# Performance work log

Measured on AMD Instinct MI355X. Metric: run time of the kernel, lower is better.

The kernel has to match this reference:

```python
import jax, jax.numpy as jnp
import numpy as np
import math
from jax import lax

DIM = 96
D_MODEL = 2 * DIM            # SS2D d_model
D_INNER = 2 * D_MODEL        # expand = 2
D_STATE = 16
DT_RANK = math.ceil(D_MODEL / 16)
K = 4
B_, H_, W_ = 2, 48, 48


def setup_inputs() -> dict:
    key = jax.random.key(0)
    ks = jax.random.split(key, 12)
    r = lambda k, s, sc=0.02: jax.random.normal(k, s, jnp.float32) * sc
    A = np.tile(np.arange(1, D_STATE + 1, dtype=np.float32)[None, :], (K * D_INNER, 1))
    return dict(
        x=jax.random.normal(ks[0], (B_, DIM, H_, W_), jnp.float32),
        w_init=r(ks[1], (D_MODEL, DIM)),
        b_init=r(ks[2], (D_MODEL,)),
        w_fina=r(ks[3], (DIM, D_MODEL)),
        b_fina=r(ks[4], (DIM,)),
        in_proj_w=r(ks[5], (2 * D_INNER, D_MODEL)),
        conv_w=r(ks[6], (D_INNER, 1, 3, 3), 0.1),
        conv_b=r(ks[7], (D_INNER,)),
        x_proj_w=r(ks[8], (K, DT_RANK + 2 * D_STATE, D_INNER)),
        dt_w=r(ks[9], (K, D_INNER, DT_RANK), 0.1),
        dt_b=r(ks[10], (K, D_INNER), 0.1),
        A_logs=jnp.asarray(np.log(A)),
        Ds=jnp.ones((K * D_INNER,), jnp.float32),
        ln_g=jnp.ones((D_INNER,), jnp.float32),
        ln_b=jnp.zeros((D_INNER,), jnp.float32),
        out_proj_w=r(ks[11], (D_MODEL, D_INNER)),
    )


def _gelu(x):
    return jax.nn.gelu(x, approximate=False)


def _conv1x1(x, w, b):
    # x: (b,c,h,w), w: (o,c)
    return jnp.einsum('oc,bchw->bohw', w, x) + b[None, :, None, None]


def _ss2d(x, in_proj_w, conv_w, conv_b, x_proj_w, dt_w, dt_b, A_logs, Ds, ln_g, ln_b, out_proj_w):
    # x: (b, h, w, d_model)
    b, h, w, _ = x.shape
    L = h * w
    xz = jnp.einsum('bhwc,oc->bhwo', x, in_proj_w)          # (b,h,w,2*d_inner)
    xx, z = jnp.split(xz, 2, axis=-1)
    xc = xx.transpose(0, 3, 1, 2)                            # (b, d_inner, h, w)
    xc = lax.conv_general_dilated(xc, conv_w, (1, 1), 'SAME',
                                  feature_group_count=D_INNER,
                                  dimension_numbers=('NCHW', 'OIHW', 'NCHW'))
    xc = jax.nn.silu(xc + conv_b[None, :, None, None])
    # 4 scan directions: hw, wh, reversed hw, reversed wh
    x_hw = xc.reshape(b, D_INNER, L)
    x_wh = xc.transpose(0, 1, 3, 2).reshape(b, D_INNER, L)
    xs = jnp.stack([x_hw, x_wh, x_hw[..., ::-1], x_wh[..., ::-1]], axis=1)   # (b,K,d,L)
    x_dbl = jnp.einsum('bkdl,kcd->bkcl', xs, x_proj_w)
    dts = x_dbl[:, :, :DT_RANK]                               # (b,K,r,L)
    Bs = x_dbl[:, :, DT_RANK:DT_RANK + D_STATE]               # (b,K,n,L)
    Cs = x_dbl[:, :, DT_RANK + D_STATE:]                      # (b,K,n,L)
    dts = jnp.einsum('bkrl,kdr->bkdl', dts, dt_w)
    delta = jax.nn.softplus(dts + dt_b[None, :, :, None])     # (b,K,d,L)
    A = -jnp.exp(A_logs).reshape(K, D_INNER, D_STATE)         # (K,d,n)
    Dm = Ds.reshape(K, D_INNER)
    # selective scan over L (time-major stacked inputs)
    u_t = xs.transpose(3, 0, 1, 2)      # (L,b,K,d)
    dt_t = delta.transpose(3, 0, 1, 2)  # (L,b,K,d)
    B_t = Bs.transpose(3, 0, 1, 2)      # (L,b,K,n)
    C_t = Cs.transpose(3, 0, 1, 2)      # (L,b,K,n)
    h0 = jnp.zeros((b, K, D_INNER, D_STATE), xs.dtype)

    def step(hst, inp):
        u, dt, Bv, Cv = inp
        dA = jnp.exp(dt[..., None] * A)                       # (b,K,d,n)
        hst = dA * hst + (dt * u)[..., None] * Bv[:, :, None, :]
        y = jnp.einsum('bkdn,bkn->bkd', hst, Cv)
        return hst, y

    _, ys = lax.scan(step, h0, (u_t, dt_t, B_t, C_t))         # (L,b,K,d)
    ys = ys.transpose(1, 2, 3, 0) + Dm[None, :, :, None] * xs  # (b,K,d,L)
    y1 = ys[:, 0]
    y3 = ys[:, 2][..., ::-1]
    y2 = ys[:, 1].reshape(b, D_INNER, w, h).transpose(0, 1, 3, 2).reshape(b, D_INNER, L)
    y4 = ys[:, 3][..., ::-1].reshape(b, D_INNER, w, h).transpose(0, 1, 3, 2).reshape(b, D_INNER, L)
    y = (y1 + y2 + y3 + y4).transpose(0, 2, 1).reshape(b, h, w, D_INNER)
    mu = y.mean(-1, keepdims=True)
    var = y.var(-1, keepdims=True)
    y = (y - mu) / jnp.sqrt(var + 1e-5) * ln_g + ln_b
    y = y * jax.nn.silu(z)
    return jnp.einsum('bhwd,od->bhwo', y, out_proj_w)         # (b,h,w,d_model)


def _forward(x, w_init, b_init, w_fina, b_fina, in_proj_w, conv_w, conv_b,
             x_proj_w, dt_w, dt_b, A_logs, Ds, ln_g, ln_b, out_proj_w):
    x1 = _gelu(_conv1x1(x, w_init, b_init))                   # (b,2*dim,h,w)
    x0 = x1
    xt = x1.transpose(0, 2, 3, 1)                             # b h w c
    y = _ss2d(xt, in_proj_w, conv_w, conv_b, x_proj_w, dt_w, dt_b,
              A_logs, Ds, ln_g, ln_b, out_proj_w)
    y = y.transpose(0, 3, 1, 2)
    return _gelu(_conv1x1(y + x0, w_fina, b_fina))            # (b,dim,h,w)


def reference(x, w_init, b_init, w_fina, b_fina, in_proj_w, conv_w, conv_b,
              x_proj_w, dt_w, dt_b, A_logs, Ds, ln_g, ln_b, out_proj_w):
    return _forward(x, w_init, b_init, w_fina, b_fina, in_proj_w, conv_w, conv_b,
                    x_proj_w, dt_w, dt_b, A_logs, Ds, ln_g, ln_b, out_proj_w)
```

## Files before the change

### kernel.cpp

```cpp
#include <hip/hip_runtime.h>
#include <math.h>

#define LL 2304
#define HH 48
#define WW 48
#define BB 2
#define CI 96
#define DM 192
#define DI 384
#define KK 4
#define RR 12
#define NN 16
#define KC 44
#define CH 96
#define LEN 24

typedef short bf16x8 __attribute__((ext_vector_type(8)));
typedef float f32x4 __attribute__((ext_vector_type(4)));

__device__ __forceinline__ float gelu_f(float x){
    return 0.5f*x*(1.0f+erff(x*0.70710678118654752f));
}
__device__ __forceinline__ float silu_f(float x){
    return x/(1.0f+__expf(-x));
}
__device__ __forceinline__ float softplus_f(float x){
    return fmaxf(x,0.0f) + log1pf(__expf(-fabsf(x)));
}
__device__ __forceinline__ unsigned short bf16_rne(float x){
    unsigned u = __float_as_uint(x);
    unsigned r = (u + 0x7FFFu + ((u>>16)&1u)) >> 16;
    return (unsigned short)r;
}
__device__ __forceinline__ void split_bf16(float x, unsigned short& h, unsigned short& l){
    h = bf16_rne(x);
    float fh = __uint_as_float(((unsigned)h)<<16);
    l = bf16_rne(x - fh);
}

template<int C, int OT>
__device__ __forceinline__ void gemmN_acc(const float* __restrict__ xb, const float* __restrict__ w,
        int o0, float* wl, float acc[OT], int tid){
    for(int idx=tid; idx<OT*C; idx+=256) wl[idx] = w[(size_t)o0*C + idx];
    __syncthreads();
    #pragma unroll 2
    for(int c=0;c<C;c+=4){
        float x0=xb[(size_t)(c+0)*LL], x1=xb[(size_t)(c+1)*LL];
        float x2=xb[(size_t)(c+2)*LL], x3=xb[(size_t)(c+3)*LL];
        #pragma unroll
        for(int o=0;o<OT;o++){
            float4 wq = *reinterpret_cast<const float4*>(wl + o*C + c);
            acc[o] = fmaf(wq.x,x0, fmaf(wq.y,x1, fmaf(wq.z,x2, fmaf(wq.w,x3, acc[o]))));
        }
    }
}

__global__ __launch_bounds__(256) void k_convw(const float* __restrict__ ipw, const float* __restrict__ xpw,
        const float* __restrict__ opw, short* __restrict__ wh_ip, short* __restrict__ wl_ip,
        short* __restrict__ wh_xp, short* __restrict__ wl_xp,
        short* __restrict__ wh_op, short* __restrict__ wl_op){
    int idx = blockIdx.x*256 + threadIdx.x;
    unsigned short h, l;
    if(idx < 147456){
        split_bf16(ipw[idx], h, l); wh_ip[idx]=h; wl_ip[idx]=l;
    } else if(idx < 147456+67584){
        int j = idx - 147456;
        split_bf16(xpw[j], h, l); wh_xp[j]=h; wl_xp[j]=l;
    } else {
        int j = idx - 215040;
        split_bf16(opw[j], h, l); wh_op[j]=h; wl_op[j]=l;
    }
}

template<int K>
__device__ __forceinline__ void mfma_core(const short* __restrict__ Ah, const short* __restrict__ Al,
        const short* __restrict__ Bh, const short* __restrict__ Bl, f32x4 acc[2][4]){
    int lane = threadIdx.x & 63;
    int rl = lane & 15, g = lane >> 4;
    #pragma unroll
    for(int kc=0; kc<K; kc+=32){
        bf16x8 ah[2], al[2], bh[4], bl[4];
        #pragma unroll
        for(int mi=0;mi<2;mi++){
            ah[mi] = *reinterpret_cast<const bf16x8*>(Ah + (size_t)(mi*16+rl)*K + kc + g*8);
            al[mi] = *reinterpret_cast<const bf16x8*>(Al + (size_t)(mi*16+rl)*K + kc + g*8);
        }
        #pragma unroll
        for(int ni=0;ni<4;ni++){
            bh[ni] = *reinterpret_cast<const bf16x8*>(Bh + (size_t)(ni*16+rl)*K + kc + g*8);
            bl[ni] = *reinterpret_cast<const bf16x8*>(Bl + (size_t)(ni*16+rl)*K + kc + g*8);
        }
        #pragma unroll
        for(int mi=0;mi<2;mi++){
            #pragma unroll
            for(int ni=0;ni<4;ni++){
                acc[mi][ni] = __builtin_amdgcn_mfma_f32_16x16x32_bf16(ah[mi], bh[ni], acc[mi][ni], 0,0,0);
                acc[mi][ni] = __builtin_amdgcn_mfma_f32_16x16x32_bf16(ah[mi], bl[ni], acc[mi][ni], 0,0,0);
                acc[mi][ni] = __builtin_amdgcn_mfma_f32_16x16x32_bf16(al[mi], bh[ni], acc[mi][ni], 0,0,0);
            }
        }
    }
}

__global__ __launch_bounds__(256) void k_init(const float* __restrict__ x, const float* __restrict__ w,
        const float* __restrict__ bias, float* __restrict__ x1,
        short* __restrict__ x1Th, short* __restrict__ x1Tl){
    __shared__ float wl[8*CI];
    int l = blockIdx.x*256 + threadIdx.x;
    int o0 = blockIdx.y*8; int b = blockIdx.z;
    float acc[8];
    #pragma unroll
    for(int j=0;j<8;j++) acc[j] = bias[o0+j];
    gemmN_acc<CI,8>(x + (size_t)b*CI*LL + l, w, o0, wl, acc, threadIdx.x);
    float* ob = x1 + (size_t)b*DM*LL + o0*LL + l;
    unsigned hw[4], lw[4];
    #pragma unroll
    for(int j=0;j<8;j+=2){
        float g0 = gelu_f(acc[j]), g1 = gelu_f(acc[j+1]);
        ob[j*LL] = g0; ob[(j+1)*LL] = g1;
        unsigned short h0,l0,h1,l1;
        split_bf16(g0,h0,l0); split_bf16(g1,h1,l1);
        hw[j>>1] = (unsigned)h0 | ((unsigned)h1<<16);
        lw[j>>1] = (unsigned)l0 | ((unsigned)l1<<16);
    }
    size_t tbase = ((size_t)b*LL + l)*DM + o0;
    *reinterpret_cast<uint4*>(x1Th + tbase) = make_uint4(hw[0],hw[1],hw[2],hw[3]);
    *reinterpret_cast<uint4*>(x1Tl + tbase) = make_uint4(lw[0],lw[1],lw[2],lw[3]);
}

__global__ __launch_bounds__(256) void k_inproj(const short* __restrict__ wh, const short* __restrict__ wlo,
        const short* __restrict__ x1Th, const short* __restrict__ x1Tl,
        float* __restrict__ xx, float* __restrict__ z){
    int w = threadIdx.x >> 6, lane = threadIdx.x & 63;
    int wm = w >> 1, wn = w & 1;
    int m0 = blockIdx.y*64 + wm*32;
    int n0 = blockIdx.x*128 + wn*64;
    int b = blockIdx.z;
    f32x4 acc[2][4];
    #pragma unroll
    for(int mi=0;mi<2;mi++)
        #pragma unroll
        for(int ni=0;ni<4;ni++) acc[mi][ni] = (f32x4){0.f,0.f,0.f,0.f};
    mfma_core<DM>(wh + (size_t)m0*DM, wlo + (size_t)m0*DM,
                  x1Th + ((size_t)b*LL + n0)*DM, x1Tl + ((size_t)b*LL + n0)*DM, acc);
    int rl = lane & 15, g = lane >> 4;
    #pragma unroll
    for(int mi=0;mi<2;mi++){
        #pragma unroll
        for(int ni=0;ni<4;ni++){
            #pragma unroll
            for(int i=0;i<4;i++){
                int m = m0 + mi*16 + g*4 + i;
                int l = n0 + ni*16 + rl;
                float v = acc[mi][ni][i];
                if(m < DI) xx[((size_t)b*DI + m)*LL + l] = v;
                else       z [((size_t)b*DI + (m-DI))*LL + l] = v;
            }
        }
    }
}

__global__ __launch_bounds__(256) void k_dwconv(const float* __restrict__ xx, const float* __restrict__ cw,
        const float* __restrict__ cb, float* __restrict__ xc){
    int l = blockIdx.x*256 + threadIdx.x;
    int d = blockIdx.y; int b = blockIdx.z;
    int h = l/WW, w = l%WW;
    const float* src = xx + ((size_t)b*DI + d)*LL;
    float acc = cb[d];
    #pragma unroll
    for(int dh=-1;dh<=1;dh++){
        int hh = h+dh; if(hh<0||hh>=HH) continue;
        #pragma unroll
        for(int dw=-1;dw<=1;dw++){
            int w2 = w+dw; if(w2<0||w2>=WW) continue;
            acc += cw[d*9 + (dh+1)*3 + (dw+1)] * src[hh*WW + w2];
        }
    }
    xc[((size_t)b*DI + d)*LL + l] = silu_f(acc);
}

__global__ __launch_bounds__(256) void k_transpose(const float* __restrict__ xc, const float* __restrict__ z,
        float* __restrict__ xcT, float* __restrict__ zT,
        short* __restrict__ xcTh, short* __restrict__ xcTl){
    __shared__ float tile[32][33];
    int which = blockIdx.z >> 1;
    int b = blockIdx.z & 1;
    const float* src = which ? z : xc;
    float* dst = which ? zT : xcT;
    int l0 = blockIdx.x*32, d0 = blockIdx.y*32;
    int tx = threadIdx.x & 31, ty = threadIdx.x >> 5;
    #pragma unroll
    for(int j=0;j<4;j++)
        tile[ty+8*j][tx] = src[((size_t)b*DI + d0+ty+8*j)*LL + l0+tx];
    __syncthreads();
    #pragma unroll
    for(int j=0;j<4;j++){
        float v = tile[tx][ty+8*j];
        size_t di = ((size_t)b*LL + l0+ty+8*j)*DI + d0+tx;
        dst[di] = v;
        if(!which){
            unsigned short h,l;
            split_bf16(v,h,l);
            xcTh[di] = (short)h; xcTl[di] = (short)l;
        }
    }
}

__global__ __launch_bounds__(256) void k_proj(const short* __restrict__ wh, const short* __restrict__ wlo,
        const short* __restrict__ xcTh, const short* __restrict__ xcTl,
        float* __restrict__ pj){
    int w = threadIdx.x >> 6, lane = threadIdx.x & 63;
    int wm = w >> 1, wn = w & 1;
    int m0 = blockIdx.y*64 + wm*32;
    int n0 = blockIdx.x*128 + wn*64;
    int b = blockIdx.z;
    f32x4 acc[2][4];
    #pragma unroll
    for(int mi=0;mi<2;mi++)
        #pragma unroll
        for(int ni=0;ni<4;ni++) acc[mi][ni] = (f32x4){0.f,0.f,0.f,0.f};
    mfma_core<DI>(wh + (size_t)m0*DI, wlo + (size_t)m0*DI,
                  xcTh + ((size_t)b*LL + n0)*DI, xcTl + ((size_t)b*LL + n0)*DI, acc);
    int rl = lane & 15, g = lane >> 4;
    #pragma unroll
    for(int mi=0;mi<2;mi++){
        #pragma unroll
        for(int ni=0;ni<4;ni++){
            #pragma unroll
            for(int i=0;i<4;i++){
                int m = m0 + mi*16 + g*4 + i;
                if(m >= KK*KC) continue;
                int l = n0 + ni*16 + rl;
                pj[((size_t)b*(KK*KC) + m)*LL + l] = acc[mi][ni][i];
            }
        }
    }
}

__global__ __launch_bounds__(256) void k_delta(const float* __restrict__ pj, const float* __restrict__ dtw,
        const float* __restrict__ dtb, float* __restrict__ deltaT){
    __shared__ float pjs[RR*32];
    int p0 = blockIdx.x*32;
    int bk = blockIdx.z; int b = bk>>2, k = bk&3;
    int lane = threadIdx.x & 63, sub = threadIdx.x >> 6;
    int d = blockIdx.y*64 + lane;
    const float* pjb = pj + ((size_t)b*(KK*KC) + k*KC)*LL;
    for(int idx=threadIdx.x; idx<RR*32; idx+=256){
        int r = idx>>5, pp = idx&31;
        pjs[idx] = pjb[(size_t)r*LL + p0+pp];
    }
    __syncthreads();
    float wr[RR];
    #pragma unroll
    for(int r=0;r<RR;r++) wr[r] = dtw[((size_t)k*DI + d)*RR + r];
    float dtbv = dtb[k*DI + d];
    #pragma unroll
    for(int i=0;i<8;i++){
        int pp = sub*8+i;
        float acc = dtbv;
        #pragma unroll
        for(int r=0;r<RR;r++) acc += wr[r]*pjs[r*32+pp];
        deltaT[((size_t)bk*LL + p0+pp)*DI + d] = softplus_f(acc);
    }
}

__device__ __forceinline__ int perm_pos(int k, int l){
    int lk = (k>=2) ? (LL-1-l) : l;
    return (k&1) ? ((lk%WW)*WW + lk/WW) : lk;
}

__global__ __launch_bounds__(384) void k_scan1(const float* __restrict__ xcT, const float* __restrict__ pj,
        const float* __restrict__ deltaT, const float* __restrict__ alogs,
        float* __restrict__ gbuf, float* __restrict__ Sbuf){
    __shared__ float bs[LEN*16];
    int chunk = blockIdx.x;
    int bk = blockIdx.y; int b = bk>>2, k = bk&3;
    int lane = threadIdx.x & 63, wv = threadIdx.x >> 6;
    int d = wv*64 + lane;
    const float* pjb = pj + ((size_t)b*(KK*KC) + k*KC)*LL;
    for(int idx=threadIdx.x; idx<LEN*16; idx+=384){
        int s = idx>>4, n = idx&15;
        int p = perm_pos(k, chunk*LEN+s);
        bs[idx] = pjb[(size_t)(RR+n)*LL + p];
    }
    __syncthreads();
    float a[NN], h[NN];
    #pragma unroll
    for(int n=0;n<NN;n++){ a[n] = -__expf(alogs[((size_t)k*DI + d)*NN + n]); h[n]=0.f; }
    float S = 0.f;
    const float* dptr = deltaT + (size_t)bk*LL*DI + d;
    const float* uptr = xcT + (size_t)b*LL*DI + d;
    for(int s=0;s<LEN;s++){
        int p = perm_pos(k, chunk*LEN+s);
        float dt = dptr[(size_t)p*DI];
        float u  = uptr[(size_t)p*DI];
        S += dt;
        float du = dt*u;
        #pragma unroll
        for(int nq=0;nq<4;nq++){
            float4 Bq = *reinterpret_cast<const float4*>(bs + s*16 + nq*4);
            h[nq*4+0] = __expf(dt*a[nq*4+0])*h[nq*4+0] + du*Bq.x;
            h[nq*4+1] = __expf(dt*a[nq*4+1])*h[nq*4+1] + du*Bq.y;
            h[nq*4+2] = __expf(dt*a[nq*4+2])*h[nq*4+2] + du*Bq.z;
            h[nq*4+3] = __expf(dt*a[nq*4+3])*h[nq*4+3] + du*Bq.w;
        }
    }
    int base = (bk*CH + chunk)*NN;
    #pragma unroll
    for(int n=0;n<NN;n++) gbuf[(size_t)(base+n)*DI + d] = h[n];
    Sbuf[(size_t)(bk*CH + chunk)*DI + d] = S;
}

__global__ __launch_bounds__(256) void k_scan2(const float* __restrict__ alogs, const float* __restrict__ Sbuf,
        float* __restrict__ gbuf){
    int id = blockIdx.x*256 + threadIdx.x;
    int d = id % DI;
    int n = (id/DI) % NN;
    int bk = id/(DI*NN);
    int k = bk & 3;
    float a = -__expf(alogs[((size_t)k*DI + d)*NN + n]);
    float h = 0.f;
    for(int j=0;j<CH;j++){
        float S = Sbuf[(size_t)(bk*CH + j)*DI + d];
        size_t gi = (size_t)((bk*CH + j)*NN + n)*DI + d;
        float g = gbuf[gi];
        gbuf[gi] = h;
        h = __expf(a*S)*h + g;
    }
}

__global__ __launch_bounds__(384) void k_scan3(const float* __restrict__ xcT, const float* __restrict__ pj,
        const float* deltaT, const float* __restrict__ alogs,
        const float* __restrict__ gbuf, float* yout){
    __shared__ float bs[LEN*32];
    int chunk = blockIdx.x;
    int bk = blockIdx.y; int b = bk>>2, k = bk&3;
    int lane = threadIdx.x & 63, wv = threadIdx.x >> 6;
    int d = wv*64 + lane;
    const float* pjb = pj + ((size_t)b*(KK*KC) + k*KC)*LL;
    for(int idx=threadIdx.x; idx<LEN*32; idx+=384){
        int s = idx>>5, c = idx&31;
        int p = perm_pos(k, chunk*LEN+s);
        bs[idx] = pjb[(size_t)(RR+c)*LL + p];
    }
    __syncthreads();
    float a[NN], h[NN];
    int base = (bk*CH + chunk)*NN;
    #pragma unroll
    for(int n=0;n<NN;n++){
        a[n] = -__expf(alogs[((size_t)k*DI + d)*NN + n]);
        h[n] = gbuf[(size_t)(base+n)*DI + d];
    }
    const float* dptr = deltaT + (size_t)bk*LL*DI + d;
    const float* uptr = xcT + (size_t)b*LL*DI + d;
    float* yptr = yout + (size_t)bk*LL*DI + d;
    for(int s=0;s<LEN;s++){
        int p = perm_pos(k, chunk*LEN+s);
        float dt = dptr[(size_t)p*DI];
        float u  = uptr[(size_t)p*DI];
        float du = dt*u;
        float y = 0.f;
        #pragma unroll
        for(int nq=0;nq<4;nq++){
            float4 Bq = *reinterpret_cast<const float4*>(bs + s*32 + nq*4);
            float4 Cq = *reinterpret_cast<const float4*>(bs + s*32 + 16 + nq*4);
            h[nq*4+0] = __expf(dt*a[nq*4+0])*h[nq*4+0] + du*Bq.x;  y += h[nq*4+0]*Cq.x;
            h[nq*4+1] = __expf(dt*a[nq*4+1])*h[nq*4+1] + du*Bq.y;  y += h[nq*4+1]*Cq.y;
            h[nq*4+2] = __expf(dt*a[nq*4+2])*h[nq*4+2] + du*Bq.z;  y += h[nq*4+2]*Cq.z;
            h[nq*4+3] = __expf(dt*a[nq*4+3])*h[nq*4+3] + du*Bq.w;  y += h[nq*4+3]*Cq.w;
        }
        yptr[(size_t)p*DI] = y;
    }
}

__global__ __launch_bounds__(256) void k_merge(const float* __restrict__ yout, const float* __restrict__ xcT,
        const float* __restrict__ zT, const float* __restrict__ Ds,
        const float* __restrict__ lng, const float* __restrict__ lnb,
        short* __restrict__ ygh, short* __restrict__ ygl){
    __shared__ float tile[32*385];
    int p0 = blockIdx.x*32; int b = blockIdx.y;
    for(int idx=threadIdx.x; idx<32*DI; idx+=256){
        int pp = idx/DI, d = idx%DI; int p = p0+pp;
        float dsum = Ds[d] + Ds[DI+d] + Ds[2*DI+d] + Ds[3*DI+d];
        float v = dsum * xcT[((size_t)b*LL + p)*DI + d];
        #pragma unroll
        for(int kk=0;kk<4;kk++) v += yout[((size_t)(b*4+kk)*LL + p)*DI + d];
        tile[pp*385 + d] = v;
    }
    __syncthreads();
    int lane = threadIdx.x & 63, wv = threadIdx.x >> 6;
    for(int i=0;i<8;i++){
        int pp = wv*8 + i; int p = p0+pp;
        float s1=0.f, s2=0.f;
        float vals[6];
        #pragma unroll
        for(int j=0;j<6;j++){ float v = tile[pp*385 + lane + 64*j]; vals[j]=v; s1+=v; s2+=v*v; }
        #pragma unroll
        for(int m=1;m<64;m<<=1){ s1 += __shfl_xor(s1,m); s2 += __shfl_xor(s2,m); }
        float mu = s1*(1.0f/DI);
        float var = s2*(1.0f/DI) - mu*mu;
        float rstd = rsqrtf(var + 1e-5f);
        #pragma unroll
        for(int j=0;j<6;j++){
            int c = lane + 64*j;
            float zv = zT[((size_t)b*LL + p)*DI + c];
            float y = (vals[j]-mu)*rstd*lng[c] + lnb[c];
            float gv = y * silu_f(zv);
            unsigned short h,l;
            split_bf16(gv,h,l);
            size_t oi = ((size_t)b*LL + p)*DI + c;
            ygh[oi] = (short)h; ygl[oi] = (short)l;
        }
    }
}

__global__ __launch_bounds__(256) void k_outproj(const short* __restrict__ wh, const short* __restrict__ wlo,
        const short* __restrict__ ygh, const short* __restrict__ ygl,
        const float* __restrict__ x1, float* __restrict__ yo){
    int w = threadIdx.x >> 6, lane = threadIdx.x & 63;
    int wm = w >> 1, wn = w & 1;
    int m0 = blockIdx.y*64 + wm*32;
    int n0 = blockIdx.x*128 + wn*64;
    int b = blockIdx.z;
    f32x4 acc[2][4];
    #pragma unroll
    for(int mi=0;mi<2;mi++)
        #pragma unroll
        for(int ni=0;ni<4;ni++) acc[mi][ni] = (f32x4){0.f,0.f,0.f,0.f};
    mfma_core<DI>(wh + (size_t)m0*DI, wlo + (size_t)m0*DI,
                  ygh + ((size_t)b*LL + n0)*DI, ygl + ((size_t)b*LL + n0)*DI, acc);
    int rl = lane & 15, g = lane >> 4;
    #pragma unroll
    for(int mi=0;mi<2;mi++){
        #pragma unroll
        for(int ni=0;ni<4;ni++){
            #pragma unroll
            for(int i=0;i<4;i++){
                int m = m0 + mi*16 + g*4 + i;
                int l = n0 + ni*16 + rl;
                size_t oi = ((size_t)b*DM + m)*LL + l;
                yo[oi] = acc[mi][ni][i] + x1[oi];
            }
        }
    }
}

__global__ __launch_bounds__(256) void k_final(const float* __restrict__ yo,
        const float* __restrict__ w, const float* __restrict__ bias, float* __restrict__ out){
    __shared__ float wl[4*DM];
    int l = blockIdx.x*256 + threadIdx.x;
    int o0 = blockIdx.y*4; int b = blockIdx.z;
    float acc[4];
    #pragma unroll
    for(int j=0;j<4;j++) acc[j] = bias[o0+j];
    gemmN_acc<DM,4>(yo + (size_t)b*DM*LL + l, w, o0, wl, acc, threadIdx.x);
    float* ob = out + (size_t)b*CI*LL + o0*LL + l;
    #pragma unroll
    for(int j=0;j<4;j++) ob[j*LL] = gelu_f(acc[j]);
}

extern "C" void kernel_launch(void* const* d_in, const int* in_sizes, int n_in,
                              void* d_out, int out_size, void* d_ws, size_t ws_size,
                              hipStream_t stream) {
    const float* x        = (const float*)d_in[0];
    const float* w_init   = (const float*)d_in[1];
    const float* b_init   = (const float*)d_in[2];
    const float* w_fina   = (const float*)d_in[3];
    const float* b_fina   = (const float*)d_in[4];
    const float* in_proj_w= (const float*)d_in[5];
    const float* conv_w   = (const float*)d_in[6];
    const float* conv_b   = (const float*)d_in[7];
    const float* x_proj_w = (const float*)d_in[8];
    const float* dt_w     = (const float*)d_in[9];
    const float* dt_b     = (const float*)d_in[10];
    const float* A_logs   = (const float*)d_in[11];
    const float* Ds       = (const float*)d_in[12];
    const float* ln_g     = (const float*)d_in[13];
    const float* ln_b     = (const float*)d_in[14];
    const float* out_proj_w=(const float*)d_in[15];

    float* ws = (float*)d_ws;
    float* x1   = ws;
    float* xx   = x1 + 884736;
    float* z    = xx + 1769472;
    float* xc   = z  + 1769472;
    float* xcT  = xc + 1769472;
    float* zT   = xcT+ 1769472;
    float* pj   = zT + 1769472;
    float* deltaT = pj + 811008;
    float* wcvt = deltaT + 7077888;

    short* wh_ip = (short*)wcvt;
    short* wl_ip = wh_ip + 147456;
    short* wh_xp = wl_ip + 147456;
    short* wl_xp = wh_xp + 73728;
    short* wh_op = wl_xp + 73728;
    short* wl_op = wh_op + 73728;

    short* x1Th = (short*)deltaT;
    short* x1Tl = x1Th + 884736;
    short* xcTh = x1Tl + 884736;
    short* xcTl = xcTh + 1769472;

    float* gbuf = xx;
    float* Sbuf = xx + 4718592;
    float* yout = deltaT;
    short* ygh  = (short*)xc;
    short* ygl  = ygh + 1769472;
    float* yo   = z;

    dim3 blk(256);
    k_convw  <<<dim3(1128), blk, 0, stream>>>(in_proj_w, x_proj_w, out_proj_w,
                                              wh_ip, wl_ip, wh_xp, wl_xp, wh_op, wl_op);
    k_init   <<<dim3(9,24,BB), blk, 0, stream>>>(x, w_init, b_init, x1, x1Th, x1Tl);
    k_inproj <<<dim3(18,12,BB), blk, 0, stream>>>(wh_ip, wl_ip, x1Th, x1Tl, xx, z);
    k_dwconv <<<dim3(9,DI,BB), blk, 0, stream>>>(xx, conv_w, conv_b, xc);
    k_transpose<<<dim3(72,12,2*BB), blk, 0, stream>>>(xc, z, xcT, zT, xcTh, xcTl);
    k_proj   <<<dim3(18,3,BB), blk, 0, stream>>>(wh_xp, wl_xp, xcTh, xcTl, pj);
    k_delta  <<<dim3(72,6,BB*KK), blk, 0, stream>>>(pj, dt_w, dt_b, deltaT);
    k_scan1  <<<dim3(CH,BB*KK), dim3(384), 0, stream>>>(xcT, pj, deltaT, A_logs, gbuf, Sbuf);
    k_scan2  <<<dim3(192), blk, 0, stream>>>(A_logs, Sbuf, gbuf);
    k_scan3  <<<dim3(CH,BB*KK), dim3(384), 0, stream>>>(xcT, pj, deltaT, A_logs, gbuf, yout);
    k_merge  <<<dim3(72,BB), blk, 0, stream>>>(yout, xcT, zT, Ds, ln_g, ln_b, ygh, ygl);
    k_outproj<<<dim3(18,3,BB), blk, 0, stream>>>(wh_op, wl_op, ygh, ygl, x1, yo);
    k_final  <<<dim3(9,24,BB), blk, 0, stream>>>(yo, w_fina, b_fina, (float*)d_out);
}
```

Baseline: 325.1 us.

## Fuse delta projection into scans and move init/final convs to split-bf16 MFMA

Removes the separate k_delta kernel and its large deltaT buffer. Each scan chunk now loads the dt-rank projection rows into shared memory and recomputes dt plus softplus inline, in both scan1 and scan3. The init and final 1x1 convolutions become split-bf16 MFMA GEMMs, using a new transpose kernel for x and having outproj write the transposed bf16 hi/lo residual sum directly. The aim is to cut memory traffic and slow fp32 FMA GEMMs, at the cost of duplicated dt work across the two scan passes, an extra launch, and a rearranged workspace.

Result: slower. 353.6 us (+8.8%).

```diff
diff --git a/kernel.cpp b/kernel.cpp
--- a/kernel.cpp
+++ b/kernel.cpp
@@ -38,37 +38,30 @@
     l = bf16_rne(x - fh);
 }
 
-template<int C, int OT>
-__device__ __forceinline__ void gemmN_acc(const float* __restrict__ xb, const float* __restrict__ w,
-        int o0, float* wl, float acc[OT], int tid){
-    for(int idx=tid; idx<OT*C; idx+=256) wl[idx] = w[(size_t)o0*C + idx];
-    __syncthreads();
-    #pragma unroll 2
-    for(int c=0;c<C;c+=4){
-        float x0=xb[(size_t)(c+0)*LL], x1=xb[(size_t)(c+1)*LL];
-        float x2=xb[(size_t)(c+2)*LL], x3=xb[(size_t)(c+3)*LL];
-        #pragma unroll
-        for(int o=0;o<OT;o++){
-            float4 wq = *reinterpret_cast<const float4*>(wl + o*C + c);
-            acc[o] = fmaf(wq.x,x0, fmaf(wq.y,x1, fmaf(wq.z,x2, fmaf(wq.w,x3, acc[o]))));
-        }
-    }
-}
-
 __global__ __launch_bounds__(256) void k_convw(const float* __restrict__ ipw, const float* __restrict__ xpw,
-        const float* __restrict__ opw, short* __restrict__ wh_ip, short* __restrict__ wl_ip,
+        const float* __restrict__ opw, const float* __restrict__ wiw, const float* __restrict__ wfw,
+        short* __restrict__ wh_ip, short* __restrict__ wl_ip,
         short* __restrict__ wh_xp, short* __restrict__ wl_xp,
-        short* __restrict__ wh_op, short* __restrict__ wl_op){
+        short* __restrict__ wh_op, short* __restrict__ wl_op,
+        short* __restrict__ wh_in, short* __restrict__ wl_in,
+        short* __restrict__ wh_fi, short* __restrict__ wl_fi){
     int idx = blockIdx.x*256 + threadIdx.x;
+    if(idx >= 325632) return;
     unsigned short h, l;
     if(idx < 147456){
         split_bf16(ipw[idx], h, l); wh_ip[idx]=h; wl_ip[idx]=l;
-    } else if(idx < 147456+67584){
+    } else if(idx < 215040){
         int j = idx - 147456;
         split_bf16(xpw[j], h, l); wh_xp[j]=h; wl_xp[j]=l;
-    } else {
+    } else if(idx < 288768){
         int j = idx - 215040;
         split_bf16(opw[j], h, l); wh_op[j]=h; wl_op[j]=l;
+    } else if(idx < 307200){
+        int j = idx - 288768;
+        split_bf16(wiw[j], h, l); wh_in[j]=h; wl_in[j]=l;
+    } else {
+        int j = idx - 307200;
+        split_bf16(wfw[j], h, l); wh_fi[j]=h; wl_fi[j]=l;
     }
 }
 
@@ -102,30 +95,63 @@
     }
 }
 
-__global__ __launch_bounds__(256) void k_init(const float* __restrict__ x, const float* __restrict__ w,
-        const float* __restrict__ bias, float* __restrict__ x1,
-        short* __restrict__ x1Th, short* __restrict__ x1Tl){
-    __shared__ float wl[8*CI];
-    int l = blockIdx.x*256 + threadIdx.x;
-    int o0 = blockIdx.y*8; int b = blockIdx.z;
-    float acc[8];
-    #pragma unroll
-    for(int j=0;j<8;j++) acc[j] = bias[o0+j];
-    gemmN_acc<CI,8>(x + (size_t)b*CI*LL + l, w, o0, wl, acc, threadIdx.x);
-    float* ob = x1 + (size_t)b*DM*LL + o0*LL + l;
-    unsigned hw[4], lw[4];
-    #pragma unroll
-    for(int j=0;j<8;j+=2){
-        float g0 = gelu_f(acc[j]), g1 = gelu_f(acc[j+1]);
-        ob[j*LL] = g0; ob[(j+1)*LL] = g1;
-        unsigned short h0,l0,h1,l1;
-        split_bf16(g0,h0,l0); split_bf16(g1,h1,l1);
-        hw[j>>1] = (unsigned)h0 | ((unsigned)h1<<16);
-        lw[j>>1] = (unsigned)l0 | ((unsigned)l1<<16);
-    }
-    size_t tbase = ((size_t)b*LL + l)*DM + o0;
-    *reinterpret_cast<uint4*>(x1Th + tbase) = make_uint4(hw[0],hw[1],hw[2],hw[3]);
-    *reinterpret_cast<uint4*>(x1Tl + tbase) = make_uint4(lw[0],lw[1],lw[2],lw[3]);
+__global__ __launch_bounds__(256) void k_xT(const float* __restrict__ x,
+        short* __restrict__ xTh, short* __restrict__ xTl){
+    __shared__ float tile[32][33];
+    int b = blockIdx.z;
+    int l0 = blockIdx.x*32, c0 = blockIdx.y*32;
+    int tx = threadIdx.x & 31, ty = threadIdx.x >> 5;
+    #pragma unroll
+    for(int j=0;j<4;j++)
+        tile[ty+8*j][tx] = x[((size_t)b*CI + c0+ty+8*j)*LL + l0+tx];
+    __syncthreads();
+    #pragma unroll
+    for(int j=0;j<4;j++){
+        float v = tile[tx][ty+8*j];
+        size_t di = ((size_t)b*LL + l0+ty+8*j)*CI + c0+tx;
+        unsigned short h,l; split_bf16(v,h,l);
+        xTh[di]=(short)h; xTl[di]=(short)l;
+    }
+}
+
+__global__ __launch_bounds__(256) void k_init(const short* __restrict__ wh, const short* __restrict__ wlo,
+        const short* __restrict__ xTh, const short* __restrict__ xTl, const float* __restrict__ bias,
+        float* __restrict__ x1, short* __restrict__ x1Th, short* __restrict__ x1Tl){
+    int w = threadIdx.x >> 6, lane = threadIdx.x & 63;
+    int wm = w >> 1, wn = w & 1;
+    int m0 = blockIdx.y*64 + wm*32;
+    int n0 = blockIdx.x*128 + wn*64;
+    int b = blockIdx.z;
+    f32x4 acc[2][4];
+    #pragma unroll
+    for(int mi=0;mi<2;mi++)
+        #pragma unroll
+        for(int ni=0;ni<4;ni++) acc[mi][ni] = (f32x4){0.f,0.f,0.f,0.f};
+    mfma_core<CI>(wh + (size_t)m0*CI, wlo + (size_t)m0*CI,
+                  xTh + ((size_t)b*LL + n0)*CI, xTl + ((size_t)b*LL + n0)*CI, acc);
+    int rl = lane & 15, g = lane >> 4;
+    #pragma unroll
+    for(int mi=0;mi<2;mi++){
+        #pragma unroll
+        for(int ni=0;ni<4;ni++){
+            int mb = m0 + mi*16 + g*4;
+            int l = n0 + ni*16 + rl;
+            unsigned hp[2], lp[2];
+            #pragma unroll
+            for(int i=0;i<4;i++){
+                int m = mb + i;
+                float v = gelu_f(acc[mi][ni][i] + bias[m]);
+                x1[((size_t)b*DM + m)*LL + l] = v;
+                unsigned short h, lo_;
+                split_bf16(v, h, lo_);
+                if(i & 1){ hp[i>>1] |= ((unsigned)h)<<16; lp[i>>1] |= ((unsigned)lo_)<<16; }
+                else     { hp[i>>1] = h; lp[i>>1] = lo_; }
+            }
+            size_t tb = ((size_t)b*LL + l)*DM + mb;
+            *reinterpret_cast<uint2*>(x1Th + tb) = make_uint2(hp[0],hp[1]);
+            *reinterpret_cast<uint2*>(x1Tl + tb) = make_uint2(lp[0],lp[1]);
+        }
+    }
 }
 
 __global__ __launch_bounds__(256) void k_inproj(const short* __restrict__ wh, const short* __restrict__ wlo,
@@ -237,42 +263,16 @@
     }
 }
 
-__global__ __launch_bounds__(256) void k_delta(const float* __restrict__ pj, const float* __restrict__ dtw,
-        const float* __restrict__ dtb, float* __restrict__ deltaT){
-    __shared__ float pjs[RR*32];
-    int p0 = blockIdx.x*32;
-    int bk = blockIdx.z; int b = bk>>2, k = bk&3;
-    int lane = threadIdx.x & 63, sub = threadIdx.x >> 6;
-    int d = blockIdx.y*64 + lane;
-    const float* pjb = pj + ((size_t)b*(KK*KC) + k*KC)*LL;
-    for(int idx=threadIdx.x; idx<RR*32; idx+=256){
-        int r = idx>>5, pp = idx&31;
-        pjs[idx] = pjb[(size_t)r*LL + p0+pp];
-    }
-    __syncthreads();
-    float wr[RR];
-    #pragma unroll
-    for(int r=0;r<RR;r++) wr[r] = dtw[((size_t)k*DI + d)*RR + r];
-    float dtbv = dtb[k*DI + d];
-    #pragma unroll
-    for(int i=0;i<8;i++){
-        int pp = sub*8+i;
-        float acc = dtbv;
-        #pragma unroll
-        for(int r=0;r<RR;r++) acc += wr[r]*pjs[r*32+pp];
-        deltaT[((size_t)bk*LL + p0+pp)*DI + d] = softplus_f(acc);
-    }
-}
-
 __device__ __forceinline__ int perm_pos(int k, int l){
     int lk = (k>=2) ? (LL-1-l) : l;
     return (k&1) ? ((lk%WW)*WW + lk/WW) : lk;
 }
 
 __global__ __launch_bounds__(384) void k_scan1(const float* __restrict__ xcT, const float* __restrict__ pj,
-        const float* __restrict__ deltaT, const float* __restrict__ alogs,
+        const float* __restrict__ dtw, const float* __restrict__ dtb, const float* __restrict__ alogs,
         float* __restrict__ gbuf, float* __restrict__ Sbuf){
     __shared__ float bs[LEN*16];
+    __shared__ float dls[LEN*RR];
     int chunk = blockIdx.x;
     int bk = blockIdx.y; int b = bk>>2, k = bk&3;
     int lane = threadIdx.x & 63, wv = threadIdx.x >> 6;
@@ -283,16 +283,27 @@
         int p = perm_pos(k, chunk*LEN+s);
         bs[idx] = pjb[(size_t)(RR+n)*LL + p];
     }
+    for(int idx=threadIdx.x; idx<LEN*RR; idx+=384){
+        int s = idx/RR, r = idx - s*RR;
+        int p = perm_pos(k, chunk*LEN+s);
+        dls[idx] = pjb[(size_t)r*LL + p];
+    }
     __syncthreads();
+    float wr[RR];
+    #pragma unroll
+    for(int r=0;r<RR;r++) wr[r] = dtw[((size_t)k*DI + d)*RR + r];
+    float dtbv = dtb[k*DI + d];
     float a[NN], h[NN];
     #pragma unroll
     for(int n=0;n<NN;n++){ a[n] = -__expf(alogs[((size_t)k*DI + d)*NN + n]); h[n]=0.f; }
     float S = 0.f;
-    const float* dptr = deltaT + (size_t)bk*LL*DI + d;
     const float* uptr = xcT + (size_t)b*LL*DI + d;
     for(int s=0;s<LEN;s++){
         int p = perm_pos(k, chunk*LEN+s);
-        float dt = dptr[(size_t)p*DI];
+        float dtraw = dtbv;
+        #pragma unroll
+        for(int r=0;r<RR;r++) dtraw += wr[r]*dls[s*RR+r];
+        float dt = softplus_f(dtraw);
         float u  = uptr[(size_t)p*DI];
         S += dt;
         float du = dt*u;
@@ -330,9 +341,10 @@
 }
 
 __global__ __launch_bounds__(384) void k_scan3(const float* __restrict__ xcT, const float* __restrict__ pj,
-        const float* deltaT, const float* __restrict__ alogs,
-        const float* __restrict__ gbuf, float* yout){
+        const float* __restrict__ dtw, const float* __restrict__ dtb, const float* __restrict__ alogs,
+        const float* __restrict__ gbuf, float* __restrict__ yout){
     __shared__ float bs[LEN*32];
+    __shared__ float dls[LEN*RR];
     int chunk = blockIdx.x;
     int bk = blockIdx.y; int b = bk>>2, k = bk&3;
     int lane = threadIdx.x & 63, wv = threadIdx.x >> 6;
@@ -343,7 +355,16 @@
         int p = perm_pos(k, chunk*LEN+s);
         bs[idx] = pjb[(size_t)(RR+c)*LL + p];
     }
+    for(int idx=threadIdx.x; idx<LEN*RR; idx+=384){
+        int s = idx/RR, r = idx - s*RR;
+        int p = perm_pos(k, chunk*LEN+s);
+        dls[idx] = pjb[(size_t)r*LL + p];
+    }
     __syncthreads();
+    float wr[RR];
+    #pragma unroll
+    for(int r=0;r<RR;r++) wr[r] = dtw[((size_t)k*DI + d)*RR + r];
+    float dtbv = dtb[k*DI + d];
     float a[NN], h[NN];
     int base = (bk*CH + chunk)*NN;
     #pragma unroll
@@ -351,12 +372,14 @@
         a[n] = -__expf(alogs[((size_t)k*DI + d)*NN + n]);
         h[n] = gbuf[(size_t)(base+n)*DI + d];
     }
-    const float* dptr = deltaT + (size_t)bk*LL*DI + d;
     const float* uptr = xcT + (size_t)b*LL*DI + d;
     float* yptr = yout + (size_t)bk*LL*DI + d;
     for(int s=0;s<LEN;s++){
         int p = perm_pos(k, chunk*LEN+s);
-        float dt = dptr[(size_t)p*DI];
+        float dtraw = dtbv;
+        #pragma unroll
+        for(int r=0;r<RR;r++) dtraw += wr[r]*dls[s*RR+r];
+        float dt = softplus_f(dtraw);
         float u  = uptr[(size_t)p*DI];
         float du = dt*u;
         float y = 0.f;
@@ -416,7 +439,7 @@
 
 __global__ __launch_bounds__(256) void k_outproj(const short* __restrict__ wh, const short* __restrict__ wlo,
         const short* __restrict__ ygh, const short* __restrict__ ygl,
-        const float* __restrict__ x1, float* __restrict__ yo){
+        const float* __restrict__ x1, short* __restrict__ yoTh, short* __restrict__ yoTl){
     int w = threadIdx.x >> 6, lane = threadIdx.x & 63;
     int wm = w >> 1, wn = w & 1;
     int m0 = blockIdx.y*64 + wm*32;
@@ -434,29 +457,54 @@
     for(int mi=0;mi<2;mi++){
         #pragma unroll
         for(int ni=0;ni<4;ni++){
+            int mb = m0 + mi*16 + g*4;
+            int l = n0 + ni*16 + rl;
+            unsigned hp[2], lp[2];
+            #pragma unroll
+            for(int i=0;i<4;i++){
+                int m = mb + i;
+                float v = acc[mi][ni][i] + x1[((size_t)b*DM + m)*LL + l];
+                unsigned short h, lo_;
+                split_bf16(v, h, lo_);
+                if(i & 1){ hp[i>>1] |= ((unsigned)h)<<16; lp[i>>1] |= ((unsigned)lo_)<<16; }
+                else     { hp[i>>1] = h; lp[i>>1] = lo_; }
+            }
+            size_t tb = ((size_t)b*LL + l)*DM + mb;
+            *reinterpret_cast<uint2*>(yoTh + tb) = make_uint2(hp[0],hp[1]);
+            *reinterpret_cast<uint2*>(yoTl + tb) = make_uint2(lp[0],lp[1]);
+        }
+    }
+}
+
+__global__ __launch_bounds__(256) void k_final(const short* __restrict__ wh, const short* __restrict__ wlo,
+        const short* __restrict__ yoTh, const short* __restrict__ yoTl, const float* __restrict__ bias,
+        float* __restrict__ out){
+    int w = threadIdx.x >> 6, lane = threadIdx.x & 63;
+    int wm = w >> 1, wn = w & 1;
+    int m0 = blockIdx.y*64 + wm*32;
+    int n0 = blockIdx.x*128 + wn*64;
+    int b = blockIdx.z;
+    f32x4 acc[2][4];
+    #pragma unroll
+    for(int mi=0;mi<2;mi++)
+        #pragma unroll
+        for(int ni=0;ni<4;ni++) acc[mi][ni] = (f32x4){0.f,0.f,0.f,0.f};
+    mfma_core<DM>(wh + (size_t)m0*DM, wlo + (size_t)m0*DM,
+                  yoTh + ((size_t)b*LL + n0)*DM, yoTl + ((size_t)b*LL + n0)*DM, acc);
+    int rl = lane & 15, g = lane >> 4;
+    #pragma unroll
+    for(int mi=0;mi<2;mi++){
+        #pragma unroll
+        for(int ni=0;ni<4;ni++){
             #pragma unroll
             for(int i=0;i<4;i++){
                 int m = m0 + mi*16 + g*4 + i;
+                if(m >= CI) continue;
                 int l = n0 + ni*16 + rl;
-                size_t oi = ((size_t)b*DM + m)*LL + l;
-                yo[oi] = acc[mi][ni][i] + x1[oi];
+                out[((size_t)b*CI + m)*LL + l] = gelu_f(acc[mi][ni][i] + bias[m]);
             }
         }
     }
-}
-
-__global__ __launch_bounds__(256) void k_final(const float* __restrict__ yo,
-        const float* __restrict__ w, const float* __restrict__ bias, float* __restrict__ out){
-    __shared__ float wl[4*DM];
-    int l = blockIdx.x*256 + threadIdx.x;
-    int o0 = blockIdx.y*4; int b = blockIdx.z;
-    float acc[4];
-    #pragma unroll
-    for(int j=0;j<4;j++) acc[j] = bias[o0+j];
-    gemmN_acc<DM,4>(yo + (size_t)b*DM*LL + l, w, o0, wl, acc, threadIdx.x);
-    float* ob = out + (size_t)b*CI*LL + o0*LL + l;
-    #pragma unroll
-    for(int j=0;j<4;j++) ob[j*LL] = gelu_f(acc[j]);
 }
 
 extern "C" void kernel_launch(void* const* d_in, const int* in_sizes, int n_in,
@@ -479,7 +527,7 @@
     const float* ln_b     = (const float*)d_in[14];
     const float* out_proj_w=(const float*)d_in[15];
 
-    float* ws = (float*)d_ws;
+    float* ws   = (float*)d_ws;
     float* x1   = ws;
     float* xx   = x1 + 884736;
     float* z    = xx + 1769472;
@@ -487,41 +535,35 @@
     float* xcT  = xc + 1769472;
     float* zT   = xcT+ 1769472;
     float* pj   = zT + 1769472;
-    float* deltaT = pj + 811008;
-    float* wcvt = deltaT + 7077888;
-
-    short* wh_ip = (short*)wcvt;
-    short* wl_ip = wh_ip + 147456;
-    short* wh_xp = wl_ip + 147456;
-    short* wl_xp = wh_xp + 73728;
-    short* wh_op = wl_xp + 73728;
-    short* wl_op = wh_op + 73728;
-
-    short* x1Th = (short*)deltaT;
-    short* x1Tl = x1Th + 884736;
-    short* xcTh = x1Tl + 884736;
-    short* xcTl = xcTh + 1769472;
-
-    float* gbuf = xx;
-    float* Sbuf = xx + 4718592;
-    float* yout = deltaT;
-    short* ygh  = (short*)xc;
-    short* ygl  = ygh + 1769472;
-    float* yo   = z;
+    float* yout = pj + 811008;
+    float* gbuf = yout + 7077888;
+    float* Sbuf = gbuf + 4718592;
+    short* sb   = (short*)(Sbuf + 294912);
+    short* wh_ip = sb;            short* wl_ip = wh_ip + 147456;
+    short* wh_xp = wl_ip+147456;  short* wl_xp = wh_xp + 73728;
+    short* wh_op = wl_xp+73728;   short* wl_op = wh_op + 73728;
+    short* wh_in = wl_op+73728;   short* wl_in = wh_in + 18432;
+    short* wh_fi = wl_in+18432;   short* wl_fi = wh_fi + 18432;
+    short* xTh   = wl_fi+18432;   short* xTl   = xTh + 442368;
+    short* x1Th  = xTl+442368;    short* x1Tl  = x1Th + 884736;
+    short* xcTh  = x1Tl+884736;   short* xcTl  = xcTh + 1769472;
+    short* ygh   = xcTl+1769472;  short* ygl   = ygh + 1769472;
+    short* yoTh  = ygl+1769472;   short* yoTl  = yoTh + 884736;
 
     dim3 blk(256);
-    k_convw  <<<dim3(1128), blk, 0, stream>>>(in_proj_w, x_proj_w, out_proj_w,
-                                              wh_ip, wl_ip, wh_xp, wl_xp, wh_op, wl_op);
-    k_init   <<<dim3(9,24,BB), blk, 0, stream>>>(x, w_init, b_init, x1, x1Th, x1Tl);
+    k_convw  <<<dim3(1272), blk, 0, stream>>>(in_proj_w, x_proj_w, out_proj_w, w_init, w_fina,
+                                              wh_ip, wl_ip, wh_xp, wl_xp, wh_op, wl_op,
+                                              wh_in, wl_in, wh_fi, wl_fi);
+    k_xT     <<<dim3(72,3,BB), blk, 0, stream>>>(x, xTh, xTl);
+    k_init   <<<dim3(18,3,BB), blk, 0, stream>>>(wh_in, wl_in, xTh, xTl, b_init, x1, x1Th, x1Tl);
     k_inproj <<<dim3(18,12,BB), blk, 0, stream>>>(wh_ip, wl_ip, x1Th, x1Tl, xx, z);
     k_dwconv <<<dim3(9,DI,BB), blk, 0, stream>>>(xx, conv_w, conv_b, xc);
     k_transpose<<<dim3(72,12,2*BB), blk, 0, stream>>>(xc, z, xcT, zT, xcTh, xcTl);
     k_proj   <<<dim3(18,3,BB), blk, 0, stream>>>(wh_xp, wl_xp, xcTh, xcTl, pj);
-    k_delta  <<<dim3(72,6,BB*KK), blk, 0, stream>>>(pj, dt_w, dt_b, deltaT);
-    k_scan1  <<<dim3(CH,BB*KK), dim3(384), 0, stream>>>(xcT, pj, deltaT, A_logs, gbuf, Sbuf);
+    k_scan1  <<<dim3(CH,BB*KK), dim3(384), 0, stream>>>(xcT, pj, dt_w, dt_b, A_logs, gbuf, Sbuf);
     k_scan2  <<<dim3(192), blk, 0, stream>>>(A_logs, Sbuf, gbuf);
-    k_scan3  <<<dim3(CH,BB*KK), dim3(384), 0, stream>>>(xcT, pj, deltaT, A_logs, gbuf, yout);
+    k_scan3  <<<dim3(CH,BB*KK), dim3(384), 0, stream>>>(xcT, pj, dt_w, dt_b, A_logs, gbuf, yout);
     k_merge  <<<dim3(72,BB), blk, 0, stream>>>(yout, xcT, zT, Ds, ln_g, ln_b, ygh, ygl);
-    k_outproj<<<dim3(18,3,BB), blk, 0, stream>>>(wh_op, wl_op, ygh, ygl, x1, yo);
-    k_final  <<<dim3(9,24,BB), blk, 0, stream>>>(yo, w_fina, b_fina, (float*)d_out);
-}
+    k_outproj<<<dim3(18,3,BB), blk, 0, stream>>>(wh_op, wl_op, ygh, ygl, x1, yoTh, yoTl);
+    k_final  <<<dim3(18,2,BB), blk, 0, stream>>>(wh_fi, wl_fi, yoTh, yoTl, b_fina, (float*)d_out);
+}
```
